# Kernel optimization log

Hardware: AMD Instinct MI355X
Metric: run time of the kernel (lower is better)

Reference implementation:

```python
import jax, jax.numpy as jnp
import numpy as np

B, S, D, H, E, K = 2, 2048, 1024, 2048, 8, 2


def setup_inputs() -> dict:
    key = jax.random.key(0)
    ks = jax.random.split(key, 9)
    sc_d = 1.0 / np.sqrt(D)
    sc_h = 1.0 / np.sqrt(H)
    return {
        "x": jax.random.normal(ks[0], (B, S, D), dtype=jnp.float32),
        "w_router": jax.random.normal(ks[1], (E, D), dtype=jnp.float32) * sc_d,
        "Wg": jax.random.normal(ks[2], (E, H, D), dtype=jnp.float32) * sc_d,  # per-expert gate proj (torch Linear weight layout [out,in])
        "Wu": jax.random.normal(ks[3], (E, H, D), dtype=jnp.float32) * sc_d,
        "Wd": jax.random.normal(ks[4], (E, D, H), dtype=jnp.float32) * sc_h,
        "sg": jax.random.normal(ks[5], (H, D), dtype=jnp.float32) * sc_d,  # shared expert
        "su": jax.random.normal(ks[6], (H, D), dtype=jnp.float32) * sc_d,
        "sd": jax.random.normal(ks[7], (D, H), dtype=jnp.float32) * sc_h,
    }


def reference(x, w_router, Wg, Wu, Wd, sg, su, sd):
    b, s, d = x.shape
    xf = x.reshape(-1, d)  # [T, D]

    # --- gating ---
    logits = jnp.einsum("td,ed->te", xf, w_router)
    probs = jax.nn.softmax(logits, axis=-1)  # [T, E]
    topw, topi = jax.lax.top_k(probs, K)  # [T, K]
    topw = topw / jnp.sum(topw, axis=-1, keepdims=True)
    # combine weights per (token, expert): topk indices are distinct per token
    comb = jnp.sum(topw[..., None] * jax.nn.one_hot(topi, E, dtype=xf.dtype), axis=1)  # [T, E]

    # --- shared expert (SwiGLU) ---
    shared = jnp.einsum(
        "th,dh->td",
        jax.nn.silu(jnp.einsum("td,hd->th", xf, sg)) * jnp.einsum("td,hd->th", xf, su),
        sd,
    )

    # --- routed experts: dense all-expert compute, weighted combine ---
    h1 = jax.nn.silu(jnp.einsum("td,ehd->teh", xf, Wg))
    h2 = jnp.einsum("td,ehd->teh", xf, Wu)
    eo = jnp.einsum("teh,edh->ted", h1 * h2, Wd)  # [T, E, D]
    routed = jnp.einsum("te,ted->td", comb, eo)

    return (routed + shared).reshape(b, s, d)
```

## Files before the change

kernel.cpp:

```cpp
#include <hip/hip_runtime.h>
#include <hip/hip_bf16.h>

#define T_TOK 4096
#define D_DIM 1024
#define H_DIM 2048

typedef __attribute__((ext_vector_type(8))) short short8;
typedef __attribute__((ext_vector_type(4))) float floatx4;

__device__ __forceinline__ unsigned short f2bf(float f) {
  unsigned int u = __builtin_bit_cast(unsigned int, f);
  return (unsigned short)((u + 0x7fffu + ((u >> 16) & 1u)) >> 16);
}

__device__ __forceinline__ void glds16(const ushort* g, ushort* l) {
  __builtin_amdgcn_global_load_lds(
      (const __attribute__((address_space(1))) unsigned int*)g,
      (__attribute__((address_space(3))) unsigned int*)l, 16, 0, 0);
}

__global__ void cvt_all_kernel(const float4* __restrict__ Wg, ushort4* __restrict__ Wgb,
                               const float4* __restrict__ Wu, ushort4* __restrict__ Wub,
                               const float4* __restrict__ Wd, ushort4* __restrict__ Wdb,
                               const float4* __restrict__ sg, ushort4* __restrict__ sgb,
                               const float4* __restrict__ su, ushort4* __restrict__ sub,
                               const float4* __restrict__ sd, ushort4* __restrict__ sdb) {
  int id = blockIdx.x;
  const float4* s; ushort4* d; int i;
  if (id < 49152) {
    int seg = id >> 14;
    int blk = id & 16383;
    s = (seg == 0) ? Wg : (seg == 1) ? Wu : Wd;
    d = (seg == 0) ? Wgb : (seg == 1) ? Wub : Wdb;
    i = blk * 256 + threadIdx.x;
  } else {
    int id2 = id - 49152;
    int seg = id2 >> 11;
    int blk = id2 & 2047;
    s = (seg == 0) ? sg : (seg == 1) ? su : sd;
    d = (seg == 0) ? sgb : (seg == 1) ? sub : sdb;
    i = blk * 256 + threadIdx.x;
  }
  float4 v = s[i];
  ushort4 o;
  o.x = f2bf(v.x); o.y = f2bf(v.y); o.z = f2bf(v.z); o.w = f2bf(v.w);
  d[i] = o;
}

__global__ void router_kernel(const float* __restrict__ x, const float* __restrict__ wr,
                              ushort* __restrict__ xb,
                              int* __restrict__ topi, float2* __restrict__ topw) {
  const int w = threadIdx.x >> 6;
  const int l = threadIdx.x & 63;
  const int t = blockIdx.x * 4 + w;
  const float4* xr = (const float4*)(x + (size_t)t * D_DIM);
  ushort4* xo = (ushort4*)(xb + (size_t)t * D_DIM);
  float p[8];
#pragma unroll
  for (int e = 0; e < 8; ++e) p[e] = 0.f;
#pragma unroll
  for (int i = 0; i < 4; ++i) {
    float4 xv = xr[i * 64 + l];
    ushort4 o;
    o.x = f2bf(xv.x); o.y = f2bf(xv.y); o.z = f2bf(xv.z); o.w = f2bf(xv.w);
    xo[i * 64 + l] = o;
#pragma unroll
    for (int e = 0; e < 8; ++e) {
      float4 wv = ((const float4*)(wr + e * D_DIM))[i * 64 + l];
      p[e] += xv.x * wv.x + xv.y * wv.y + xv.z * wv.z + xv.w * wv.w;
    }
  }
#pragma unroll
  for (int off = 32; off > 0; off >>= 1) {
#pragma unroll
    for (int e = 0; e < 8; ++e) p[e] += __shfl_xor(p[e], off, 64);
  }
  if (l == 0) {
    float mx = p[0];
#pragma unroll
    for (int e = 1; e < 8; ++e) mx = fmaxf(mx, p[e]);
    float pr[8];
#pragma unroll
    for (int e = 0; e < 8; ++e) pr[e] = __expf(p[e] - mx);
    int i0 = 0;
#pragma unroll
    for (int e = 1; e < 8; ++e) if (pr[e] > pr[i0]) i0 = e;
    int i1 = (i0 == 0) ? 1 : 0;
#pragma unroll
    for (int e = 0; e < 8; ++e) if (e != i0 && pr[e] > pr[i1]) i1 = e;
    float w0 = pr[i0], w1 = pr[i1];
    float inv = 1.f / (w0 + w1);
    topi[t] = i0 | (i1 << 8);
    topw[t] = make_float2(w0 * inv, w1 * inv);
  }
}

__global__ void build_lists_kernel(const int* __restrict__ topi, const float2* __restrict__ topw,
                                   int* __restrict__ counts, int* __restrict__ list,
                                   float* __restrict__ wlist) {
  const int e = blockIdx.x;
  const int tid = threadIdx.x;
  const int l = tid & 63;
  const int w = tid >> 6;
  __shared__ int wtot[4];
  int base = 0;
  for (int c = 0; c < T_TOK; c += 256) {
    int t = c + tid;
    int ti = topi[t];
    int e0 = ti & 255, e1 = ti >> 8;
    bool flag = (e0 == e) || (e1 == e);
    float2 tw = topw[t];
    float wv = (e0 == e) ? tw.x : tw.y;
    unsigned long long m = __ballot(flag);
    int lanepos = __popcll(m & ((1ull << l) - 1ull));
    if (l == 0) wtot[w] = __popcll(m);
    __syncthreads();
    int waveoff = 0;
#pragma unroll
    for (int i = 0; i < 4; ++i) waveoff += (i < w) ? wtot[i] : 0;
    int tot = wtot[0] + wtot[1] + wtot[2] + wtot[3];
    if (flag) {
      int p = base + waveoff + lanepos;
      list[e * T_TOK + p] = t;
      wlist[e * T_TOK + p] = wv;
    }
    base += tot;
    __syncthreads();
  }
  if (tid == 0) counts[e] = base;
}

__global__ void offsets_kernel(const int* __restrict__ counts, int* __restrict__ offs) {
  if (threadIdx.x == 0) {
    int acc = 0;
    for (int e = 0; e < 8; ++e) { offs[e] = acc; acc += counts[e]; }
    offs[8] = acc;
  }
}

__global__ __launch_bounds__(256, 2)
void gemm1_kernel(const ushort* __restrict__ xb,
                  const ushort* __restrict__ Wgb, const ushort* __restrict__ Wub,
                  const ushort* __restrict__ sgb, const ushort* __restrict__ sub,
                  const int* __restrict__ list,
                  const int* __restrict__ counts, const int* __restrict__ offs,
                  ushort* __restrict__ h) {
  const int e = blockIdx.z;
  const int n_e = (e == 8) ? T_TOK : counts[e];
  const int r0 = blockIdx.y * 128;
  if (r0 >= n_e) return;
  const int c0 = blockIdx.x * 128;
  const ushort* Wg = (e == 8) ? sgb : (Wgb + (size_t)e * H_DIM * D_DIM);
  const ushort* Wu = (e == 8) ? sub : (Wub + (size_t)e * H_DIM * D_DIM);
  const int hrow0 = offs[e] + r0;

  __shared__ __align__(16) ushort As[128 * 64];
  __shared__ __align__(16) ushort Bgs[128 * 64];
  __shared__ __align__(16) ushort Bus[128 * 64];
  __shared__ int toks[128];

  const int tid = threadIdx.x;
  const int l = tid & 63;
  const int w = tid >> 6;

  if (tid < 128) {
    int rr = r0 + tid;
    toks[tid] = (e == 8) ? ((rr < T_TOK) ? rr : (T_TOK - 1))
                         : list[e * T_TOK + ((rr < n_e) ? rr : (n_e - 1))];
  }
  __syncthreads();

  const int lrow8 = l >> 3;
  const int csw = (((l & 7) ^ lrow8) << 3);
  const ushort* ap[4];
#pragma unroll
  for (int i = 0; i < 4; ++i) {
    int ri = (w * 4 + i) * 8 + lrow8;
    ap[i] = xb + (size_t)toks[ri] * D_DIM + csw;
  }
  const ushort* bgp = Wg + (size_t)(c0 + w * 32 + lrow8) * D_DIM + csw;
  const ushort* bup = Wu + (size_t)(c0 + w * 32 + lrow8) * D_DIM + csw;

  floatx4 accg[4][4], accu[4][4];
#pragma unroll
  for (int i = 0; i < 4; ++i)
#pragma unroll
    for (int j = 0; j < 4; ++j) {
      accg[i][j] = (floatx4)(0.f);
      accu[i][j] = (floatx4)(0.f);
    }

  const int mrow = (w & 1) * 64;
  const int ncol = (w >> 1) * 64;
  int rba[4], rbb[4];
#pragma unroll
  for (int i = 0; i < 4; ++i) {
    rba[i] = (mrow + 16 * i + (l & 15)) * 64;
    rbb[i] = (ncol + 16 * i + (l & 15)) * 64;
  }

  for (int k0 = 0; k0 < D_DIM; k0 += 64) {
    __syncthreads();
#pragma unroll
    for (int i = 0; i < 4; ++i) {
      glds16(ap[i] + k0,                As  + (w * 4 + i) * 512);
      glds16(bgp + k0 + i * 8 * D_DIM,  Bgs + (w * 4 + i) * 512);
      glds16(bup + k0 + i * 8 * D_DIM,  Bus + (w * 4 + i) * 512);
    }
    __syncthreads();
#pragma unroll
    for (int s = 0; s < 2; ++s) {
      const int pq = ((((s << 2) | (l >> 4)) ^ (l & 7)) << 3);
      short8 a[4], bg[4], bu[4];
#pragma unroll
      for (int i = 0; i < 4; ++i) a[i] = *(const short8*)(As + rba[i] + pq);
#pragma unroll
      for (int j = 0; j < 4; ++j) {
        bg[j] = *(const short8*)(Bgs + rbb[j] + pq);
        bu[j] = *(const short8*)(Bus + rbb[j] + pq);
      }
#pragma unroll
      for (int i = 0; i < 4; ++i)
#pragma unroll
        for (int j = 0; j < 4; ++j) {
          accg[i][j] = __builtin_amdgcn_mfma_f32_16x16x32_bf16(a[i], bg[j], accg[i][j], 0, 0, 0);
          accu[i][j] = __builtin_amdgcn_mfma_f32_16x16x32_bf16(a[i], bu[j], accu[i][j], 0, 0, 0);
        }
    }
  }

#pragma unroll
  for (int i = 0; i < 4; ++i) {
#pragma unroll
    for (int r = 0; r < 4; ++r) {
      int lrow = mrow + 16 * i + (l >> 4) * 4 + r;
      if (r0 + lrow < n_e) {
#pragma unroll
        for (int j = 0; j < 4; ++j) {
          float g = accg[i][j][r];
          float u = accu[i][j][r];
          float hv = (g / (1.f + __expf(-g))) * u;
          int col = c0 + ncol + 16 * j + (l & 15);
          h[(size_t)(hrow0 + lrow) * H_DIM + col] = f2bf(hv);
        }
      }
    }
  }
}

__global__ __launch_bounds__(256, 3)
void gemm2_kernel(const ushort* __restrict__ h,
                  const ushort* __restrict__ Wdb, const ushort* __restrict__ sdb,
                  const int* __restrict__ list, const float* __restrict__ wlist,
                  const int* __restrict__ counts, const int* __restrict__ offs,
                  float* __restrict__ out) {
  const int e = blockIdx.z;
  const int n_e = (e == 8) ? T_TOK : counts[e];
  const int r0 = blockIdx.y * 128;
  if (r0 >= n_e) return;
  const int c0 = blockIdx.x * 128;
  const ushort* Wd = (e == 8) ? sdb : (Wdb + (size_t)e * D_DIM * H_DIM);
  const int hrow0 = offs[e] + r0;

  __shared__ __align__(16) ushort As[128 * 64];
  __shared__ __align__(16) ushort Bs[128 * 64];
  __shared__ int toks[128];
  __shared__ float wts[128];

  const int tid = threadIdx.x;
  const int l = tid & 63;
  const int w = tid >> 6;

  if (tid < 128) {
    int rr = r0 + tid;
    if (e == 8) {
      toks[tid] = (rr < T_TOK) ? rr : (T_TOK - 1);
      wts[tid] = 1.0f;
    } else {
      int idx = (rr < n_e) ? rr : (n_e - 1);
      toks[tid] = list[e * T_TOK + idx];
      wts[tid] = (rr < n_e) ? wlist[e * T_TOK + idx] : 0.f;
    }
  }

  const int lrow8 = l >> 3;
  const int csw = (((l & 7) ^ lrow8) << 3);
  const ushort* apb = h  + (size_t)(hrow0 + w * 32 + lrow8) * H_DIM + csw;
  const ushort* bpb = Wd + (size_t)(c0 + w * 32 + lrow8) * H_DIM + csw;

  floatx4 acc[4][4];
#pragma unroll
  for (int i = 0; i < 4; ++i)
#pragma unroll
    for (int j = 0; j < 4; ++j) acc[i][j] = (floatx4)(0.f);

  const int mrow = (w & 1) * 64;
  const int ncol = (w >> 1) * 64;
  int rba[4], rbb[4];
#pragma unroll
  for (int i = 0; i < 4; ++i) {
    rba[i] = (mrow + 16 * i + (l & 15)) * 64;
    rbb[i] = (ncol + 16 * i + (l & 15)) * 64;
  }

  for (int k0 = 0; k0 < H_DIM; k0 += 64) {
    __syncthreads();
#pragma unroll
    for (int i = 0; i < 4; ++i) {
      glds16(apb + k0 + i * 8 * H_DIM, As + (w * 4 + i) * 512);
      glds16(bpb + k0 + i * 8 * H_DIM, Bs + (w * 4 + i) * 512);
    }
    __syncthreads();
#pragma unroll
    for (int s = 0; s < 2; ++s) {
      const int pq = ((((s << 2) | (l >> 4)) ^ (l & 7)) << 3);
      short8 a[4], b[4];
#pragma unroll
      for (int i = 0; i < 4; ++i) a[i] = *(const short8*)(As + rba[i] + pq);
#pragma unroll
      for (int j = 0; j < 4; ++j) b[j] = *(const short8*)(Bs + rbb[j] + pq);
#pragma unroll
      for (int i = 0; i < 4; ++i)
#pragma unroll
        for (int j = 0; j < 4; ++j)
          acc[i][j] = __builtin_amdgcn_mfma_f32_16x16x32_bf16(a[i], b[j], acc[i][j], 0, 0, 0);
    }
  }

#pragma unroll
  for (int i = 0; i < 4; ++i) {
#pragma unroll
    for (int r = 0; r < 4; ++r) {
      int lrow = mrow + 16 * i + (l >> 4) * 4 + r;
      if (r0 + lrow < n_e) {
        int tok = toks[lrow];
        float wt = wts[lrow];
#pragma unroll
        for (int j = 0; j < 4; ++j) {
          int col = c0 + ncol + 16 * j + (l & 15);
          atomicAdd(&out[(size_t)tok * D_DIM + col], wt * acc[i][j][r]);
        }
      }
    }
  }
}

#define OFF_XB   0ull
#define OFF_WGB  (OFF_XB + 8388608ull)
#define OFF_WUB  (OFF_WGB + 33554432ull)
#define OFF_WDB  (OFF_WUB + 33554432ull)
#define OFF_SGB  (OFF_WDB + 33554432ull)
#define OFF_SUB  (OFF_SGB + 4194304ull)
#define OFF_SDB  (OFF_SUB + 4194304ull)
#define OFF_H    (OFF_SDB + 4194304ull)
#define OFF_CNT  (OFF_H + 50331648ull)
#define OFF_OFFS (OFF_CNT + 64ull)
#define OFF_LIST (OFF_OFFS + 64ull)
#define OFF_WLST (OFF_LIST + 131072ull)
#define OFF_TOPI (OFF_WLST + 131072ull)
#define OFF_TOPW (OFF_TOPI + 16384ull)

extern "C" void kernel_launch(void* const* d_in, const int* in_sizes, int n_in,
                              void* d_out, int out_size, void* d_ws, size_t ws_size,
                              hipStream_t stream) {
  const float* x  = (const float*)d_in[0];
  const float* wr = (const float*)d_in[1];
  const float* Wg = (const float*)d_in[2];
  const float* Wu = (const float*)d_in[3];
  const float* Wd = (const float*)d_in[4];
  const float* sg = (const float*)d_in[5];
  const float* su = (const float*)d_in[6];
  const float* sd = (const float*)d_in[7];
  float* out = (float*)d_out;
  char* ws = (char*)d_ws;

  ushort* xb  = (ushort*)(ws + OFF_XB);
  ushort* Wgb = (ushort*)(ws + OFF_WGB);
  ushort* Wub = (ushort*)(ws + OFF_WUB);
  ushort* Wdb = (ushort*)(ws + OFF_WDB);
  ushort* sgb = (ushort*)(ws + OFF_SGB);
  ushort* sub = (ushort*)(ws + OFF_SUB);
  ushort* sdb = (ushort*)(ws + OFF_SDB);
  ushort* hbuf = (ushort*)(ws + OFF_H);
  int* counts = (int*)(ws + OFF_CNT);
  int* offs   = (int*)(ws + OFF_OFFS);
  int* list   = (int*)(ws + OFF_LIST);
  float* wlist = (float*)(ws + OFF_WLST);
  int* topi   = (int*)(ws + OFF_TOPI);
  float2* topw = (float2*)(ws + OFF_TOPW);

  hipMemsetAsync(d_out, 0, (size_t)out_size * sizeof(float), stream);

  cvt_all_kernel<<<55296, 256, 0, stream>>>((const float4*)Wg, (ushort4*)Wgb,
                                            (const float4*)Wu, (ushort4*)Wub,
                                            (const float4*)Wd, (ushort4*)Wdb,
                                            (const float4*)sg, (ushort4*)sgb,
                                            (const float4*)su, (ushort4*)sub,
                                            (const float4*)sd, (ushort4*)sdb);

  router_kernel<<<1024, 256, 0, stream>>>(x, wr, xb, topi, topw);
  build_lists_kernel<<<8, 256, 0, stream>>>(topi, topw, counts, list, wlist);
  offsets_kernel<<<1, 64, 0, stream>>>(counts, offs);

  gemm1_kernel<<<dim3(16, 32, 9), 256, 0, stream>>>(xb, Wgb, Wub, sgb, sub,
                                                    list, counts, offs, hbuf);
  gemm2_kernel<<<dim3(8, 32, 9), 256, 0, stream>>>(hbuf, Wdb, sdb,
                                                   list, wlist, counts, offs, out);
}
```

Measured before the change: 481.2 us.

## Replace atomic scatter with bf16 expert outputs and gather-combine kernel; fuse Wd conversion

```diff
diff --git a/kernel.cpp b/kernel.cpp
--- a/kernel.cpp
+++ b/kernel.cpp
@@ -11,6 +11,11 @@
 __device__ __forceinline__ unsigned short f2bf(float f) {
   unsigned int u = __builtin_bit_cast(unsigned int, f);
   return (unsigned short)((u + 0x7fffu + ((u >> 16) & 1u)) >> 16);
+}
+
+__device__ __forceinline__ float bf2f(unsigned short s) {
+  unsigned int u = ((unsigned int)s) << 16;
+  return __builtin_bit_cast(float, u);
 }
 
 __device__ __forceinline__ void glds16(const ushort* g, ushort* l) {
@@ -19,28 +24,16 @@
       (__attribute__((address_space(3))) unsigned int*)l, 16, 0, 0);
 }
 
-__global__ void cvt_all_kernel(const float4* __restrict__ Wg, ushort4* __restrict__ Wgb,
-                               const float4* __restrict__ Wu, ushort4* __restrict__ Wub,
-                               const float4* __restrict__ Wd, ushort4* __restrict__ Wdb,
-                               const float4* __restrict__ sg, ushort4* __restrict__ sgb,
-                               const float4* __restrict__ su, ushort4* __restrict__ sub,
-                               const float4* __restrict__ sd, ushort4* __restrict__ sdb) {
-  int id = blockIdx.x;
+__global__ void cvt_kernel(const float4* __restrict__ Wg, ushort4* __restrict__ Wgb,
+                           const float4* __restrict__ Wu, ushort4* __restrict__ Wub,
+                           const float4* __restrict__ sg, ushort4* __restrict__ sgb,
+                           const float4* __restrict__ su, ushort4* __restrict__ sub) {
+  int id = blockIdx.x * 256 + threadIdx.x;
   const float4* s; ushort4* d; int i;
-  if (id < 49152) {
-    int seg = id >> 14;
-    int blk = id & 16383;
-    s = (seg == 0) ? Wg : (seg == 1) ? Wu : Wd;
-    d = (seg == 0) ? Wgb : (seg == 1) ? Wub : Wdb;
-    i = blk * 256 + threadIdx.x;
-  } else {
-    int id2 = id - 49152;
-    int seg = id2 >> 11;
-    int blk = id2 & 2047;
-    s = (seg == 0) ? sg : (seg == 1) ? su : sd;
-    d = (seg == 0) ? sgb : (seg == 1) ? sub : sdb;
-    i = blk * 256 + threadIdx.x;
-  }
+  if (id < 4194304)      { s = Wg; d = Wgb; i = id; }
+  else if (id < 8388608) { s = Wu; d = Wub; i = id - 4194304; }
+  else if (id < 8912896) { s = sg; d = sgb; i = id - 8388608; }
+  else                   { s = su; d = sub; i = id - 8912896; }
   float4 v = s[i];
   ushort4 o;
   o.x = f2bf(v.x); o.y = f2bf(v.y); o.z = f2bf(v.z); o.w = f2bf(v.w);
@@ -95,9 +88,9 @@
   }
 }
 
-__global__ void build_lists_kernel(const int* __restrict__ topi, const float2* __restrict__ topw,
+__global__ void build_lists_kernel(const int* __restrict__ topi,
                                    int* __restrict__ counts, int* __restrict__ list,
-                                   float* __restrict__ wlist) {
+                                   int* __restrict__ pos) {
   const int e = blockIdx.x;
   const int tid = threadIdx.x;
   const int l = tid & 63;
@@ -109,8 +102,6 @@
     int ti = topi[t];
     int e0 = ti & 255, e1 = ti >> 8;
     bool flag = (e0 == e) || (e1 == e);
-    float2 tw = topw[t];
-    float wv = (e0 == e) ? tw.x : tw.y;
     unsigned long long m = __ballot(flag);
     int lanepos = __popcll(m & ((1ull << l) - 1ull));
     if (l == 0) wtot[w] = __popcll(m);
@@ -122,44 +113,69 @@
     if (flag) {
       int p = base + waveoff + lanepos;
       list[e * T_TOK + p] = t;
-      wlist[e * T_TOK + p] = wv;
+      int slot = (e0 == e) ? 0 : 1;
+      pos[t * 2 + slot] = p;
     }
     base += tot;
     __syncthreads();
   }
   if (tid == 0) counts[e] = base;
-}
-
-__global__ void offsets_kernel(const int* __restrict__ counts, int* __restrict__ offs) {
-  if (threadIdx.x == 0) {
-    int acc = 0;
-    for (int e = 0; e < 8; ++e) { offs[e] = acc; acc += counts[e]; }
-    offs[8] = acc;
-  }
 }
 
 __global__ __launch_bounds__(256, 2)
 void gemm1_kernel(const ushort* __restrict__ xb,
                   const ushort* __restrict__ Wgb, const ushort* __restrict__ Wub,
                   const ushort* __restrict__ sgb, const ushort* __restrict__ sub,
-                  const int* __restrict__ list,
-                  const int* __restrict__ counts, const int* __restrict__ offs,
+                  const float4* __restrict__ Wd, ushort4* __restrict__ Wdb,
+                  const float4* __restrict__ sd, ushort4* __restrict__ sdb,
+                  const int* __restrict__ list, const int* __restrict__ counts,
                   ushort* __restrict__ h) {
+  const int tid = threadIdx.x;
+  {
+    int bid = blockIdx.x + 16 * blockIdx.y + 512 * blockIdx.z;
+#pragma unroll
+    for (int it = 0; it < 4; ++it) {
+      int idx = (bid * 4 + it) * 256 + tid;
+      if (idx < 4194304) {
+        float4 v = Wd[idx];
+        ushort4 o;
+        o.x = f2bf(v.x); o.y = f2bf(v.y); o.z = f2bf(v.z); o.w = f2bf(v.w);
+        Wdb[idx] = o;
+      }
+    }
+    if (bid < 2048) {
+      int idx = bid * 256 + tid;
+      float4 v = sd[idx];
+      ushort4 o;
+      o.x = f2bf(v.x); o.y = f2bf(v.y); o.z = f2bf(v.z); o.w = f2bf(v.w);
+      sdb[idx] = o;
+    }
+  }
+
   const int e = blockIdx.z;
-  const int n_e = (e == 8) ? T_TOK : counts[e];
+  int n_e, hbase;
+  {
+    int acc = 0, ce = 0;
+    for (int q = 0; q < 8; ++q) {
+      int c = counts[q];
+      if (q < e) acc += c;
+      if (q == e) ce = c;
+    }
+    n_e = (e == 8) ? T_TOK : ce;
+    hbase = (e == 8) ? 8192 : acc;
+  }
   const int r0 = blockIdx.y * 128;
   if (r0 >= n_e) return;
   const int c0 = blockIdx.x * 128;
   const ushort* Wg = (e == 8) ? sgb : (Wgb + (size_t)e * H_DIM * D_DIM);
   const ushort* Wu = (e == 8) ? sub : (Wub + (size_t)e * H_DIM * D_DIM);
-  const int hrow0 = offs[e] + r0;
+  const int hrow0 = hbase + r0;
 
   __shared__ __align__(16) ushort As[128 * 64];
   __shared__ __align__(16) ushort Bgs[128 * 64];
   __shared__ __align__(16) ushort Bus[128 * 64];
   __shared__ int toks[128];
 
-  const int tid = threadIdx.x;
   const int l = tid & 63;
   const int w = tid >> 6;
 
@@ -251,37 +267,32 @@
 __global__ __launch_bounds__(256, 3)
 void gemm2_kernel(const ushort* __restrict__ h,
                   const ushort* __restrict__ Wdb, const ushort* __restrict__ sdb,
-                  const int* __restrict__ list, const float* __restrict__ wlist,
-                  const int* __restrict__ counts, const int* __restrict__ offs,
-                  float* __restrict__ out) {
+                  const int* __restrict__ counts,
+                  ushort* __restrict__ eo) {
   const int e = blockIdx.z;
-  const int n_e = (e == 8) ? T_TOK : counts[e];
+  int n_e, hbase;
+  {
+    int acc = 0, ce = 0;
+    for (int q = 0; q < 8; ++q) {
+      int c = counts[q];
+      if (q < e) acc += c;
+      if (q == e) ce = c;
+    }
+    n_e = (e == 8) ? T_TOK : ce;
+    hbase = (e == 8) ? 8192 : acc;
+  }
   const int r0 = blockIdx.y * 128;
   if (r0 >= n_e) return;
   const int c0 = blockIdx.x * 128;
   const ushort* Wd = (e == 8) ? sdb : (Wdb + (size_t)e * D_DIM * H_DIM);
-  const int hrow0 = offs[e] + r0;
+  const int hrow0 = hbase + r0;
 
   __shared__ __align__(16) ushort As[128 * 64];
   __shared__ __align__(16) ushort Bs[128 * 64];
-  __shared__ int toks[128];
-  __shared__ float wts[128];
 
   const int tid = threadIdx.x;
   const int l = tid & 63;
   const int w = tid >> 6;
-
-  if (tid < 128) {
-    int rr = r0 + tid;
-    if (e == 8) {
-      toks[tid] = (rr < T_TOK) ? rr : (T_TOK - 1);
-      wts[tid] = 1.0f;
-    } else {
-      int idx = (rr < n_e) ? rr : (n_e - 1);
-      toks[tid] = list[e * T_TOK + idx];
-      wts[tid] = (rr < n_e) ? wlist[e * T_TOK + idx] : 0.f;
-    }
-  }
 
   const int lrow8 = l >> 3;
   const int csw = (((l & 7) ^ lrow8) << 3);
@@ -333,16 +344,42 @@
     for (int r = 0; r < 4; ++r) {
       int lrow = mrow + 16 * i + (l >> 4) * 4 + r;
       if (r0 + lrow < n_e) {
-        int tok = toks[lrow];
-        float wt = wts[lrow];
 #pragma unroll
         for (int j = 0; j < 4; ++j) {
           int col = c0 + ncol + 16 * j + (l & 15);
-          atomicAdd(&out[(size_t)tok * D_DIM + col], wt * acc[i][j][r]);
+          eo[(size_t)(hrow0 + lrow) * D_DIM + col] = f2bf(acc[i][j][r]);
         }
       }
     }
   }
+}
+
+__global__ void combine_kernel(const ushort* __restrict__ eo, const int* __restrict__ topi,
+                               const float2* __restrict__ topw, const int* __restrict__ pos,
+                               const int* __restrict__ counts, float* __restrict__ out) {
+  const int t = blockIdx.x;
+  const int c4 = threadIdx.x;
+  int ti = topi[t];
+  int e0 = ti & 255, e1 = ti >> 8;
+  int off0 = 0, off1 = 0;
+#pragma unroll
+  for (int q = 0; q < 8; ++q) {
+    int c = counts[q];
+    off0 += (q < e0) ? c : 0;
+    off1 += (q < e1) ? c : 0;
+  }
+  float2 wv = topw[t];
+  int2 p = ((const int2*)pos)[t];
+  const ushort4* ra = (const ushort4*)(eo + (size_t)(off0 + p.x) * D_DIM);
+  const ushort4* rb = (const ushort4*)(eo + (size_t)(off1 + p.y) * D_DIM);
+  const ushort4* rs = (const ushort4*)(eo + (size_t)(8192 + t) * D_DIM);
+  ushort4 a = ra[c4], b = rb[c4], s = rs[c4];
+  float4 o;
+  o.x = wv.x * bf2f(a.x) + wv.y * bf2f(b.x) + bf2f(s.x);
+  o.y = wv.x * bf2f(a.y) + wv.y * bf2f(b.y) + bf2f(s.y);
+  o.z = wv.x * bf2f(a.z) + wv.y * bf2f(b.z) + bf2f(s.z);
+  o.w = wv.x * bf2f(a.w) + wv.y * bf2f(b.w) + bf2f(s.w);
+  ((float4*)(out + (size_t)t * D_DIM))[c4] = o;
 }
 
 #define OFF_XB   0ull
@@ -353,11 +390,11 @@
 #define OFF_SUB  (OFF_SGB + 4194304ull)
 #define OFF_SDB  (OFF_SUB + 4194304ull)
 #define OFF_H    (OFF_SDB + 4194304ull)
+#define OFF_EO   OFF_WGB
 #define OFF_CNT  (OFF_H + 50331648ull)
-#define OFF_OFFS (OFF_CNT + 64ull)
-#define OFF_LIST (OFF_OFFS + 64ull)
-#define OFF_WLST (OFF_LIST + 131072ull)
-#define OFF_TOPI (OFF_WLST + 131072ull)
+#define OFF_LIST (OFF_CNT + 64ull)
+#define OFF_POS  (OFF_LIST + 131072ull)
+#define OFF_TOPI (OFF_POS + 32768ull)
 #define OFF_TOPW (OFF_TOPI + 16384ull)
 
 extern "C" void kernel_launch(void* const* d_in, const int* in_sizes, int n_in,
@@ -382,28 +419,25 @@
   ushort* sub = (ushort*)(ws + OFF_SUB);
   ushort* sdb = (ushort*)(ws + OFF_SDB);
   ushort* hbuf = (ushort*)(ws + OFF_H);
+  ushort* eo   = (ushort*)(ws + OFF_EO);
   int* counts = (int*)(ws + OFF_CNT);
-  int* offs   = (int*)(ws + OFF_OFFS);
   int* list   = (int*)(ws + OFF_LIST);
-  float* wlist = (float*)(ws + OFF_WLST);
+  int* pos    = (int*)(ws + OFF_POS);
   int* topi   = (int*)(ws + OFF_TOPI);
   float2* topw = (float2*)(ws + OFF_TOPW);
 
-  hipMemsetAsync(d_out, 0, (size_t)out_size * sizeof(float), stream);
-
-  cvt_all_kernel<<<55296, 256, 0, stream>>>((const float4*)Wg, (ushort4*)Wgb,
-                                            (const float4*)Wu, (ushort4*)Wub,
-                                            (const float4*)Wd, (ushort4*)Wdb,
-                                            (const float4*)sg, (ushort4*)sgb,
-                                            (const float4*)su, (ushort4*)sub,
-                                            (const float4*)sd, (ushort4*)sdb);
+  cvt_kernel<<<36864, 256, 0, stream>>>((const float4*)Wg, (ushort4*)Wgb,
+                                        (const float4*)Wu, (ushort4*)Wub,
+                                        (const float4*)sg, (ushort4*)sgb,
+                                        (const float4*)su, (ushort4*)sub);
 
   router_kernel<<<1024, 256, 0, stream>>>(x, wr, xb, topi, topw);
-  build_lists_kernel<<<8, 256, 0, stream>>>(topi, topw, counts, list, wlist);
-  offsets_kernel<<<1, 64, 0, stream>>>(counts, offs);
+  build_lists_kernel<<<8, 256, 0, stream>>>(topi, counts, list, pos);
 
   gemm1_kernel<<<dim3(16, 32, 9), 256, 0, stream>>>(xb, Wgb, Wub, sgb, sub,
-                                                    list, counts, offs, hbuf);
-  gemm2_kernel<<<dim3(8, 32, 9), 256, 0, stream>>>(hbuf, Wdb, sdb,
-                                                   list, wlist, counts, offs, out);
-}
+                                                    (const float4*)Wd, (ushort4*)Wdb,
+                                                    (const float4*)sd, (ushort4*)sdb,
+                                                    list, counts, hbuf);
+  gemm2_kernel<<<dim3(8, 32, 9), 256, 0, stream>>>(hbuf, Wdb, sdb, counts, eo);
+  combine_kernel<<<4096, 256, 0, stream>>>(eo, topi, topw, pos, counts, out);
+}
```

Result: no change. 475.8 us (-1.1%).
